# Performance work log

Hardware: AMD Instinct MI355X
Metric: run time of the kernel (lower is better)

The kernel has to match this reference:

```python
import jax, jax.numpy as jnp
import numpy as np

N_NODES = 100_000
M_EDGES = 500_000
F = 128       # elem_fea_len
H = 3         # elem_heads
HD = 256      # hidden layer dim of gate/message nets
BN_EPS = 1e-5


def setup_inputs() -> dict:
    key = jax.random.key(0)
    ks = jax.random.split(key, 12)
    s = 0.05
    return {
        "elem_weights": jax.random.uniform(ks[0], (N_NODES, 1), jnp.float32, 0.05, 1.0),
        "elem_in_fea": jax.random.normal(ks[1], (N_NODES, F), jnp.float32),
        "gate_W1": jax.random.normal(ks[2], (H, 2 * F, HD), jnp.float32) * s,
        "gate_b1": jnp.zeros((H, HD), jnp.float32),
        "gate_g": jnp.ones((H, HD), jnp.float32),
        "gate_beta": jnp.zeros((H, HD), jnp.float32),
        "gate_Wo": jax.random.normal(ks[3], (H, HD, 1), jnp.float32) * s,
        "gate_bo": jnp.zeros((H, 1), jnp.float32),
        "msg_W1": jax.random.normal(ks[4], (H, 2 * F, HD), jnp.float32) * s,
        "msg_b1": jnp.zeros((H, HD), jnp.float32),
        "msg_g": jnp.ones((H, HD), jnp.float32),
        "msg_beta": jnp.zeros((H, HD), jnp.float32),
        "msg_Wo": jax.random.normal(ks[5], (H, HD, F), jnp.float32) * s,
        "msg_bo": jnp.zeros((H, F), jnp.float32),
        "pow_p": jax.random.normal(ks[6], (H, 1), jnp.float32),
        "self_fea_idx": jax.random.randint(ks[7], (M_EDGES,), 0, N_NODES, jnp.int32),
        "nbr_fea_idx": jax.random.randint(ks[8], (M_EDGES,), 0, N_NODES, jnp.int32),
    }


def _simple_net(x, W1, b1, g, beta, Wo, bo):
    # Linear -> BatchNorm1d (training-mode batch stats) -> SiLU -> Linear
    h = x @ W1 + b1
    mu = jnp.mean(h, axis=0)
    var = jnp.mean(jnp.square(h - mu), axis=0)  # biased var, as torch BN
    h = (h - mu) * jax.lax.rsqrt(var + BN_EPS) * g + beta
    h = jax.nn.silu(h)
    return h @ Wo + bo


def reference(elem_weights, elem_in_fea, gate_W1, gate_b1, gate_g, gate_beta,
              gate_Wo, gate_bo, msg_W1, msg_b1, msg_g, msg_beta, msg_Wo,
              msg_bo, pow_p, self_fea_idx, nbr_fea_idx):
    n = elem_in_fea.shape[0]
    # gather edge endpoint features: (M, 2F)
    fea = jnp.concatenate([elem_in_fea[self_fea_idx], elem_in_fea[nbr_fea_idx]], axis=1)
    w = elem_weights[nbr_fea_idx]  # (M, 1)

    def head(gW1, gb1, gg, gbe, gWo, gbo, mW1, mb1, mg, mbe, mWo, mbo, p):
        gate = _simple_net(fea, gW1, gb1, gg, gbe, gWo, gbo)          # (M, 1)
        gmax = jax.ops.segment_max(gate, self_fea_idx, num_segments=n)
        gate = (w ** p) * jnp.exp(gate - gmax[self_fea_idx])
        den = jax.ops.segment_sum(gate, self_fea_idx, num_segments=n)
        gate = gate / (den[self_fea_idx] + 1e-10)
        msg = _simple_net(fea, mW1, mb1, mg, mbe, mWo, mbo)           # (M, F)
        return jax.ops.segment_sum(gate * msg, self_fea_idx, num_segments=n)

    head_out = jax.vmap(head)(gate_W1, gate_b1, gate_g, gate_beta, gate_Wo,
                              gate_bo, msg_W1, msg_b1, msg_g, msg_beta,
                              msg_Wo, msg_bo, pow_p)                  # (H, N, F)
    return jnp.mean(head_out, axis=0) + elem_in_fea
```

## Files before the change

### kernel.cpp

```cpp
#include <hip/hip_runtime.h>
#include <stdint.h>

#define NN 100000
#define MM 500000
#define FD 128
#define KK 256
#define NHEADS 3
#define NTILES 3907

typedef __attribute__((ext_vector_type(8))) __bf16 bf16x8;
typedef __attribute__((ext_vector_type(4))) float floatx4;

__device__ __forceinline__ float bf2f(unsigned short u) {
    union { uint32_t i; float f; } c; c.i = ((uint32_t)u) << 16; return c.f;
}
__device__ __forceinline__ unsigned short f2bf(float f) {
    union { float f; uint32_t i; } c; c.f = f;
    uint32_t i = c.i;
    return (unsigned short)((i + 0x7FFFu + ((i >> 16) & 1u)) >> 16);
}
__device__ __forceinline__ unsigned short f2bf_hw(float f) {
    __bf16 h = (__bf16)f;
    return __builtin_bit_cast(unsigned short, h);
}
__device__ __forceinline__ float silu(float a) { return a / (1.f + __expf(-a)); }
__device__ __forceinline__ float fin(float v) {
    return (v == v && fabsf(v) < 1e30f) ? v : 0.f;
}

__global__ void k_zero(float* __restrict__ p, int nwords) {
    int i = blockIdx.x * 256 + threadIdx.x;
    if (i < nwords) p[i] = 0.f;
}

__global__ void k_castx(const float* __restrict__ x, unsigned short* __restrict__ xb) {
    int i = blockIdx.x * 256 + threadIdx.x;
    if (i < NN * FD / 2) {
        float2 v = ((const float2*)x)[i];
        uint32_t p = (uint32_t)f2bf(v.x) | ((uint32_t)f2bf(v.y) << 16);
        ((uint32_t*)xb)[i] = p;
    }
}

__global__ void k_transpose_w1(const float* __restrict__ gw1,
                               const float* __restrict__ mw1,
                               unsigned short* __restrict__ W1t) {
    int idx = blockIdx.x * 256 + threadIdx.x;
    int j = idx >> 16;
    int rem = idx & 65535;
    int n = rem >> 8, k = rem & 255;
    const float* src = (j < 3) ? (gw1 + (size_t)j * 65536)
                               : (mw1 + (size_t)(j - 3) * 65536);
    W1t[(size_t)idx] = f2bf(src[k * 256 + n]);
}
__global__ void k_transpose_wo(const float* __restrict__ mwo,
                               unsigned short* __restrict__ Wot) {
    int idx = blockIdx.x * 256 + threadIdx.x;
    int h = idx / 32768;
    int rem = idx % 32768;
    int f = rem >> 8, k = rem & 255;
    Wot[idx] = f2bf(mwo[(size_t)h * 32768 + k * 128 + f]);
}

__global__ void k_hist(const int* __restrict__ idx, int* __restrict__ cnt) {
    int e = blockIdx.x * 256 + threadIdx.x;
    if (e < MM) atomicAdd(&cnt[idx[e]], 1);
}
__global__ void k_scan1(const int* __restrict__ cnt, int* __restrict__ pincl, int* __restrict__ bsum) {
    __shared__ int s[256];
    int t = threadIdx.x;
    int i = blockIdx.x * 256 + t;
    int v = (i < NN) ? cnt[i] : 0;
    s[t] = v; __syncthreads();
    for (int o = 1; o < 256; o <<= 1) {
        int add = (t >= o) ? s[t - o] : 0;
        __syncthreads();
        s[t] += add;
        __syncthreads();
    }
    if (i < NN) pincl[i] = s[t];
    if (t == 255) bsum[blockIdx.x] = s[255];
}
__global__ void k_scan2(const int* __restrict__ bsum, int* __restrict__ boff, int nb) {
    __shared__ int s[512];
    int t = threadIdx.x;
    int v = (t < nb) ? bsum[t] : 0;
    s[t] = v; __syncthreads();
    for (int o = 1; o < 512; o <<= 1) {
        int add = (t >= o) ? s[t - o] : 0;
        __syncthreads();
        s[t] += add;
        __syncthreads();
    }
    if (t < nb) boff[t] = s[t] - v;
}
__global__ void k_scan3(const int* __restrict__ pincl, const int* __restrict__ boff, int* __restrict__ rp) {
    int i = blockIdx.x * 256 + threadIdx.x;
    if (i < NN) rp[i + 1] = pincl[i] + boff[i >> 8];
    if (i == 0) rp[0] = 0;
}
__global__ void k_scatter(const int* __restrict__ self, const int* __restrict__ rp,
                          int* __restrict__ fill, int* __restrict__ elist) {
    int e = blockIdx.x * 256 + threadIdx.x;
    if (e < MM) {
        int n = self[e];
        int pos = atomicAdd(&fill[n], 1);
        elist[rp[n] + pos] = e;
    }
}
__global__ void k_perm(const int* __restrict__ elist, const int* __restrict__ self,
                       const int* __restrict__ nbr, int* __restrict__ selfp, int* __restrict__ nbrp) {
    int i = blockIdx.x * 256 + threadIdx.x;
    if (i < MM) {
        int e = elist[i];
        selfp[i] = self[e];
        nbrp[i] = nbr[e];
    }
}

__global__ void k_colsum(const float* __restrict__ x,
                         const int* __restrict__ cnt_self, const int* __restrict__ cnt_nbr,
                         float* __restrict__ colsum) {
    int t = threadIdx.x;
    int col = t & 127, part = t >> 7;
    const int* cp = part ? cnt_nbr : cnt_self;
    int n0 = blockIdx.x * 512;
    float a = 0.f;
    for (int i = 0; i < 512; i++) {
        int n = n0 + i;
        if (n < NN) {
            float c = (float)cp[n];
            a += c * x[(size_t)n * FD + col];
        }
    }
    atomicAdd(&colsum[part * 128 + col], a);
}

#define NCH 7813
#define CPB 62
__global__ __launch_bounds__(256, 2)
void k_S(const unsigned short* __restrict__ xb,
         const int* __restrict__ self_idx, const int* __restrict__ nbr_idx,
         float* __restrict__ S) {
    __shared__ unsigned short LT[256][72];
    const int tid = threadIdx.x;
    const int e_l = tid & 63;
    const int half = tid >> 6;
    const int ti = blockIdx.y >> 1, tj = blockIdx.y & 1;
    const int lane = tid & 63, w = tid >> 6;
    const int lr = lane & 15, q = lane >> 4;

    int cbeg = blockIdx.x * CPB;
    int cend = cbeg + CPB; if (cend > NCH) cend = NCH;

    floatx4 acc[2][8];
#pragma unroll
    for (int a = 0; a < 2; a++)
#pragma unroll
        for (int b = 0; b < 8; b++)
#pragma unroll
            for (int r = 0; r < 4; r++) acc[a][b][r] = 0.f;

    for (int ch = cbeg; ch < cend; ch++) {
        int e = ch * 64 + e_l;
        union { uint4 v[8]; unsigned short us[64]; } buf;
        if (e < MM) {
            int node = (half < 2) ? self_idx[e] : nbr_idx[e];
            const unsigned short* src = xb + (size_t)node * FD + (half & 1) * 64;
#pragma unroll
            for (int u2 = 0; u2 < 8; u2++) buf.v[u2] = *(const uint4*)(src + u2 * 8);
        } else {
#pragma unroll
            for (int u2 = 0; u2 < 8; u2++) { buf.v[u2].x = 0u; buf.v[u2].y = 0u; buf.v[u2].z = 0u; buf.v[u2].w = 0u; }
        }
        __syncthreads();
#pragma unroll
        for (int j2 = 0; j2 < 64; j2++)
            LT[half * 64 + j2][e_l] = buf.us[j2];
        __syncthreads();
#pragma unroll
        for (int ks = 0; ks < 64; ks += 32) {
            bf16x8 aF[2], bF[8];
#pragma unroll
            for (int mi = 0; mi < 2; mi++)
                aF[mi] = *(const bf16x8*)&LT[ti * 128 + w * 32 + mi * 16 + lr][ks + q * 8];
#pragma unroll
            for (int nj = 0; nj < 8; nj++)
                bF[nj] = *(const bf16x8*)&LT[tj * 128 + nj * 16 + lr][ks + q * 8];
#pragma unroll
            for (int mi = 0; mi < 2; mi++)
#pragma unroll
                for (int nj = 0; nj < 8; nj++)
                    acc[mi][nj] = __builtin_amdgcn_mfma_f32_16x16x32_bf16(aF[mi], bF[nj], acc[mi][nj], 0, 0, 0);
        }
    }
#pragma unroll
    for (int mi = 0; mi < 2; mi++)
#pragma unroll
        for (int nj = 0; nj < 8; nj++)
#pragma unroll
            for (int r = 0; r < 4; r++) {
                int row = ti * 128 + w * 32 + mi * 16 + q * 4 + r;
                int col = tj * 128 + nj * 16 + lr;
                atomicAdd(&S[row * 256 + col], acc[mi][nj][r]);
            }
}

__global__ void k_stats(const float* __restrict__ S, const float* __restrict__ colsum,
                        const unsigned short* __restrict__ W1t,
                        const float* __restrict__ gg, const float* __restrict__ gbe,
                        const float* __restrict__ mg, const float* __restrict__ mbe,
                        float* __restrict__ scaleA, float* __restrict__ shiftA) {
    __shared__ float ws[16][257];
    __shared__ float qq[16], uu[16];
    int t = threadIdx.x;
    int j = blockIdx.y;
    int c0 = blockIdx.x * 16;
    const unsigned short* Wn = W1t + (size_t)j * 65536;
    const float* g    = (j < 3) ? gg + j * 256 : mg + (j - 3) * 256;
    const float* beta = (j < 3) ? gbe + j * 256 : mbe + (j - 3) * 256;
#pragma unroll
    for (int i = 0; i < 16; i++) ws[i][t] = bf2f(Wn[(size_t)(c0 + i) * 256 + t]);
    if (t < 16) { qq[t] = 0.f; uu[t] = 0.f; }
    __syncthreads();
    float vpart[16];
#pragma unroll
    for (int i = 0; i < 16; i++) vpart[i] = 0.f;
    for (int k = 0; k < 256; k++) {
        float s = S[k * 256 + t];
#pragma unroll
        for (int i = 0; i < 16; i++) vpart[i] += s * ws[i][k];
    }
    float cs = colsum[t];
    int lane = t & 63;
#pragma unroll
    for (int i = 0; i < 16; i++) {
        float q1 = ws[i][t] * vpart[i];
        float u1 = cs * ws[i][t];
#pragma unroll
        for (int m = 1; m <= 32; m <<= 1) { q1 += __shfl_xor(q1, m); u1 += __shfl_xor(u1, m); }
        if (lane == 0) { atomicAdd(&qq[i], q1); atomicAdd(&uu[i], u1); }
    }
    __syncthreads();
    if (t < 16) {
        int c = c0 + t;
        float mu = fin(uu[t] / (float)MM);
        float var = fmaxf(fin(qq[t] / (float)MM - mu * mu), 0.f);
        float sc = fin(g[c] * rsqrtf(var + 1e-5f));
        scaleA[j * 256 + c] = sc;
        shiftA[j * 256 + c] = fin(beta[c] - mu * sc);
    }
}

__global__ __launch_bounds__(256, 2)
void k_gate(const unsigned short* __restrict__ x,
            const int* __restrict__ selfp, const int* __restrict__ nbrp,
            const unsigned short* __restrict__ W1t,
            const float* __restrict__ scale, const float* __restrict__ shift,
            const float* __restrict__ wo, const float* __restrict__ bo,
            float* __restrict__ glog) {
    __shared__ unsigned short As[128][72];
    __shared__ unsigned short Bs[128][72];
    __shared__ float sc[3][256], sh[3][256], wv[3][256];

    const int tid = threadIdx.x;
    const int m0 = blockIdx.x * 128;
#pragma unroll
    for (int h = 0; h < 3; h++) {
        sc[h][tid] = scale[h * 256 + tid];
        sh[h][tid] = shift[h * 256 + tid];
        wv[h][tid] = wo[h * 256 + tid];
    }
    __syncthreads();

    const int lane = tid & 63, w = tid >> 6;
    const int lr = lane & 15, q = lane >> 4;
    const int r0 = tid >> 1, hf = tid & 1;

    const int e0 = m0 + r0;
    const bool ein = e0 < MM;
    const int nodeS = ein ? selfp[e0] : 0;
    const int nodeN = ein ? nbrp[e0] : 0;
    const unsigned short* srcS = x + (size_t)nodeS * FD;
    const unsigned short* srcN = x + (size_t)nodeN * FD;

    for (int h = 0; h < 3; h++) {
        const unsigned short* W1h = W1t + (size_t)h * 65536;
        float dotp[2][4];
#pragma unroll
        for (int mi = 0; mi < 2; mi++)
#pragma unroll
            for (int r = 0; r < 4; r++) dotp[mi][r] = 0.f;

        for (int nh = 0; nh < 2; nh++) {
            floatx4 acc[2][8];
#pragma unroll
            for (int a = 0; a < 2; a++)
#pragma unroll
                for (int b = 0; b < 8; b++)
#pragma unroll
                    for (int r = 0; r < 4; r++) acc[a][b][r] = 0.f;

            for (int kc = 0; kc < 4; kc++) {
                {
                    const unsigned short* src = ((kc < 2) ? srcS : srcN) + (kc & 1) * 64 + hf * 32;
#pragma unroll
                    for (int u = 0; u < 4; u++)
                        *(uint4*)&As[r0][hf * 32 + u * 8] = *(const uint4*)(src + u * 8);
                }
                {
                    const unsigned short* src = W1h + (size_t)(nh * 128 + r0) * KK + kc * 64 + hf * 32;
#pragma unroll
                    for (int u = 0; u < 4; u++)
                        *(uint4*)&Bs[r0][hf * 32 + u * 8] = *(const uint4*)(src + u * 8);
                }
                __syncthreads();
#pragma unroll
                for (int ks = 0; ks < 64; ks += 32) {
                    bf16x8 aF[2], bF[8];
#pragma unroll
                    for (int mi = 0; mi < 2; mi++)
                        aF[mi] = *(const bf16x8*)&As[w * 32 + mi * 16 + lr][ks + q * 8];
#pragma unroll
                    for (int nj = 0; nj < 8; nj++)
                        bF[nj] = *(const bf16x8*)&Bs[nj * 16 + lr][ks + q * 8];
#pragma unroll
                    for (int mi = 0; mi < 2; mi++)
#pragma unroll
                        for (int nj = 0; nj < 8; nj++)
                            acc[mi][nj] = __builtin_amdgcn_mfma_f32_16x16x32_bf16(aF[mi], bF[nj], acc[mi][nj], 0, 0, 0);
                }
                __syncthreads();
            }
#pragma unroll
            for (int mi = 0; mi < 2; mi++)
#pragma unroll
                for (int r = 0; r < 4; r++) {
                    float d = 0.f;
#pragma unroll
                    for (int nj = 0; nj < 8; nj++) {
                        int cg = nh * 128 + nj * 16 + lr;
                        float v = acc[mi][nj][r] * sc[h][cg] + sh[h][cg];
                        d += silu(v) * wv[h][cg];
                    }
                    dotp[mi][r] += d;
                }
        }
        float b0 = bo[h];
#pragma unroll
        for (int mi = 0; mi < 2; mi++)
#pragma unroll
            for (int r = 0; r < 4; r++) {
                float v = dotp[mi][r];
                v += __shfl_xor(v, 1); v += __shfl_xor(v, 2);
                v += __shfl_xor(v, 4); v += __shfl_xor(v, 8);
                if (lr == 0) {
                    int row = w * 32 + mi * 16 + q * 4 + r;
                    int e = m0 + row;
                    if (e < MM) glog[(size_t)h * MM + e] = fin(v + b0);
                }
            }
    }
}

__global__ void k_coef(const int* __restrict__ rp, const float* __restrict__ glog,
                       float* __restrict__ coef, const float* __restrict__ ew,
                       const int* __restrict__ nbrp, const float* __restrict__ powp) {
    int n = blockIdx.x * 256 + threadIdx.x;
    if (n >= NN) return;
    int b = rp[n], e = rp[n + 1];
    if (e <= b) return;
    for (int h = 0; h < NHEADS; h++) {
        const float* gl = glog + (size_t)h * MM;
        float* cf = coef + (size_t)h * MM;
        float p = powp[h];
        float gmax = -3.4e38f;
        for (int i = b; i < e; i++) gmax = fmaxf(gmax, gl[i]);
        float den = 0.f;
        for (int i = b; i < e; i++) {
            float wv = ew[nbrp[i]];
            float u = fin(powf(wv, p) * __expf(gl[i] - gmax));
            cf[i] = u; den += u;
        }
        float inv = fin(1.f / (den + 1e-10f));
        for (int i = b; i < e; i++) cf[i] = fin(cf[i] * inv);
    }
}

__global__ __launch_bounds__(256, 2)
void k_msg(const unsigned short* __restrict__ x,
           const int* __restrict__ selfp, const int* __restrict__ nbrp,
           const unsigned short* __restrict__ W1t,
           const float* __restrict__ scale, const float* __restrict__ shift,
           const unsigned short* __restrict__ Wo2t,
           const float* __restrict__ bo2,
           const float* __restrict__ coef,
           float* __restrict__ out_acc) {
    __shared__ unsigned short As[128][72];
    __shared__ unsigned short Bs[128][72];
    __shared__ unsigned short ActC[128][72];
    __shared__ float sc[3][256], sh[3][256];
    __shared__ float bvec[3][128], cfs[3][128];
    __shared__ int nid[128];

    const int tid = threadIdx.x;
    const int m0 = blockIdx.x * 128;
#pragma unroll
    for (int h = 0; h < 3; h++) {
        sc[h][tid] = scale[h * 256 + tid];
        sh[h][tid] = shift[h * 256 + tid];
    }
    if (tid < 128) {
        int e = m0 + tid;
        nid[tid] = (e < MM) ? selfp[e] : -1;
#pragma unroll
        for (int h = 0; h < 3; h++) {
            bvec[h][tid] = bo2[h * 128 + tid];
            cfs[h][tid] = (e < MM) ? coef[(size_t)h * MM + e] : 0.f;
        }
    }
    __syncthreads();

    const int lane = tid & 63, w = tid >> 6;
    const int lr = lane & 15, q = lane >> 4;
    const int r0 = tid >> 1, hf = tid & 1;

    const int e0 = m0 + r0;
    const bool ein = e0 < MM;
    const int nodeS = ein ? selfp[e0] : 0;
    const int nodeN = ein ? nbrp[e0] : 0;
    const unsigned short* srcS = x + (size_t)nodeS * FD;
    const unsigned short* srcN = x + (size_t)nodeN * FD;

    floatx4 acc2[2][8];
#pragma unroll
    for (int a = 0; a < 2; a++)
#pragma unroll
        for (int b = 0; b < 8; b++)
#pragma unroll
            for (int r = 0; r < 4; r++) acc2[a][b][r] = 0.f;

    for (int h = 0; h < 3; h++) {
        const unsigned short* W1h = W1t + (size_t)h * 65536;
        const unsigned short* Wo2h = Wo2t + (size_t)h * 32768;
        float cfr[2][4];
#pragma unroll
        for (int mi = 0; mi < 2; mi++)
#pragma unroll
            for (int r = 0; r < 4; r++) cfr[mi][r] = cfs[h][w * 32 + mi * 16 + q * 4 + r];

        for (int nh = 0; nh < 2; nh++) {
            floatx4 acc[2][8];
#pragma unroll
            for (int a = 0; a < 2; a++)
#pragma unroll
                for (int b = 0; b < 8; b++)
#pragma unroll
                    for (int r = 0; r < 4; r++) acc[a][b][r] = 0.f;

            for (int kc = 0; kc < 4; kc++) {
                {
                    const unsigned short* src = ((kc < 2) ? srcS : srcN) + (kc & 1) * 64 + hf * 32;
#pragma unroll
                    for (int u = 0; u < 4; u++)
                        *(uint4*)&As[r0][hf * 32 + u * 8] = *(const uint4*)(src + u * 8);
                }
                {
                    const unsigned short* src = W1h + (size_t)(nh * 128 + r0) * KK + kc * 64 + hf * 32;
#pragma unroll
                    for (int u = 0; u < 4; u++)
                        *(uint4*)&Bs[r0][hf * 32 + u * 8] = *(const uint4*)(src + u * 8);
                }
                __syncthreads();
#pragma unroll
                for (int ks = 0; ks < 64; ks += 32) {
                    bf16x8 aF[2], bF[8];
#pragma unroll
                    for (int mi = 0; mi < 2; mi++)
                        aF[mi] = *(const bf16x8*)&As[w * 32 + mi * 16 + lr][ks + q * 8];
#pragma unroll
                    for (int nj = 0; nj < 8; nj++)
                        bF[nj] = *(const bf16x8*)&Bs[nj * 16 + lr][ks + q * 8];
#pragma unroll
                    for (int mi = 0; mi < 2; mi++)
#pragma unroll
                        for (int nj = 0; nj < 8; nj++)
                            acc[mi][nj] = __builtin_amdgcn_mfma_f32_16x16x32_bf16(aF[mi], bF[nj], acc[mi][nj], 0, 0, 0);
                }
                __syncthreads();
            }
            for (int kc2 = 0; kc2 < 2; kc2++) {
#pragma unroll
                for (int mi = 0; mi < 2; mi++)
#pragma unroll
                    for (int njl = 0; njl < 4; njl++)
#pragma unroll
                        for (int r = 0; r < 4; r++) {
                            int nj = kc2 * 4 + njl;
                            int row = w * 32 + mi * 16 + q * 4 + r;
                            int cg = nh * 128 + nj * 16 + lr;
                            float v = acc[mi][nj][r] * sc[h][cg] + sh[h][cg];
                            ActC[row][njl * 16 + lr] = f2bf_hw(silu(v) * cfr[mi][r]);
                        }
                {
                    const unsigned short* src = Wo2h + (size_t)r0 * KK + nh * 128 + kc2 * 64 + hf * 32;
#pragma unroll
                    for (int u = 0; u < 4; u++)
                        *(uint4*)&Bs[r0][hf * 32 + u * 8] = *(const uint4*)(src + u * 8);
                }
                __syncthreads();
#pragma unroll
                for (int ks = 0; ks < 64; ks += 32) {
                    bf16x8 aF[2], bF[8];
#pragma unroll
                    for (int mi = 0; mi < 2; mi++)
                        aF[mi] = *(const bf16x8*)&ActC[w * 32 + mi * 16 + lr][ks + q * 8];
#pragma unroll
                    for (int nj = 0; nj < 8; nj++)
                        bF[nj] = *(const bf16x8*)&Bs[nj * 16 + lr][ks + q * 8];
#pragma unroll
                    for (int mi = 0; mi < 2; mi++)
#pragma unroll
                        for (int nj = 0; nj < 8; nj++)
                            acc2[mi][nj] = __builtin_amdgcn_mfma_f32_16x16x32_bf16(aF[mi], bF[nj], acc2[mi][nj], 0, 0, 0);
                }
                __syncthreads();
            }
        }
    }
#pragma unroll
    for (int mi = 0; mi < 2; mi++) {
        int rbase = w * 32 + mi * 16 + q * 4;
        int n0 = nid[rbase], n3 = nid[rbase + 3];
        float c0[3], c1[3], c2[3], c3[3];
#pragma unroll
        for (int h = 0; h < 3; h++) {
            c0[h] = cfs[h][rbase];     c1[h] = cfs[h][rbase + 1];
            c2[h] = cfs[h][rbase + 2]; c3[h] = cfs[h][rbase + 3];
        }
#pragma unroll
        for (int nj = 0; nj < 8; nj++) {
            int col = nj * 16 + lr;
            float b0h = bvec[0][col], b1h = bvec[1][col], b2h = bvec[2][col];
            float v0 = acc2[mi][nj][0] + c0[0] * b0h + c0[1] * b1h + c0[2] * b2h;
            float v1 = acc2[mi][nj][1] + c1[0] * b0h + c1[1] * b1h + c1[2] * b2h;
            float v2 = acc2[mi][nj][2] + c2[0] * b0h + c2[1] * b1h + c2[2] * b2h;
            float v3 = acc2[mi][nj][3] + c3[0] * b0h + c3[1] * b1h + c3[2] * b2h;
            if (n0 == n3) {
                if (n0 >= 0) atomicAdd(&out_acc[(size_t)n0 * FD + col], v0 + v1 + v2 + v3);
            } else {
                int n1 = nid[rbase + 1], n2 = nid[rbase + 2];
                if (n0 >= 0) atomicAdd(&out_acc[(size_t)n0 * FD + col], v0);
                if (n1 >= 0) atomicAdd(&out_acc[(size_t)n1 * FD + col], v1);
                if (n2 >= 0) atomicAdd(&out_acc[(size_t)n2 * FD + col], v2);
                if (n3 >= 0) atomicAdd(&out_acc[(size_t)n3 * FD + col], v3);
            }
        }
    }
}

__global__ void k_finalout(float* __restrict__ out, const float* __restrict__ x) {
    int i = blockIdx.x * 256 + threadIdx.x;
    if (i < NN * FD) out[i] = fin(out[i]) * (1.f / 3.f) + x[i];
}

extern "C" void kernel_launch(void* const* d_in, const int* in_sizes, int n_in,
                              void* d_out, int out_size, void* d_ws, size_t ws_size,
                              hipStream_t stream) {
    const float* ew   = (const float*)d_in[0];
    const float* x    = (const float*)d_in[1];
    const float* gW1  = (const float*)d_in[2];
    const float* gg   = (const float*)d_in[4];
    const float* gbe  = (const float*)d_in[5];
    const float* gWo  = (const float*)d_in[6];
    const float* gbo  = (const float*)d_in[7];
    const float* mW1  = (const float*)d_in[8];
    const float* mg   = (const float*)d_in[10];
    const float* mbe  = (const float*)d_in[11];
    const float* mWo  = (const float*)d_in[12];
    const float* mbo  = (const float*)d_in[13];
    const float* powp = (const float*)d_in[14];
    const int* self_idx = (const int*)d_in[15];
    const int* nbr_idx  = (const int*)d_in[16];
    float* out = (float*)d_out;

    char* ws = (char*)d_ws;
    size_t off = 0;
    auto alloc = [&](size_t bytes) -> void* {
        size_t o = off;
        off += (bytes + 255) & ~(size_t)255;
        return (void*)(ws + o);
    };

    float* S       = (float*)alloc(256 * 256 * 4);
    float* colsum  = (float*)alloc(512 * 4);
    int*   cnt     = (int*)alloc((size_t)NN * 4);
    int*   cntn    = (int*)alloc((size_t)NN * 4);
    int*   fill    = (int*)alloc((size_t)NN * 4);
    size_t zero_end = off;
    unsigned short* xb   = (unsigned short*)alloc((size_t)NN * FD * 2);
    unsigned short* W1t  = (unsigned short*)alloc(6ull * 65536 * 2);
    unsigned short* Wo2t = (unsigned short*)alloc(3ull * 32768 * 2);
    float* scaleA = (float*)alloc(6ull * 256 * 4);
    float* shiftA = (float*)alloc(6ull * 256 * 4);
    int*   rp     = (int*)alloc((size_t)(NN + 1) * 4);
    int*   pincl  = (int*)alloc((size_t)NN * 4);
    int*   bsum   = (int*)alloc(512 * 4);
    int*   boff   = (int*)alloc(512 * 4);
    int*   elist  = (int*)alloc((size_t)MM * 4);
    int*   selfp  = (int*)alloc((size_t)MM * 4);
    int*   nbrp   = (int*)alloc((size_t)MM * 4);
    float* glog   = (float*)alloc(3ull * MM * 4);
    float* coef   = (float*)alloc(3ull * MM * 4);
    if (off > ws_size) return;

    int zwords = (int)(zero_end / 4);
    k_zero<<<(zwords + 255) / 256, 256, 0, stream>>>(S, zwords);
    k_zero<<<(NN * FD + 255) / 256, 256, 0, stream>>>(out, NN * FD);

    k_castx<<<(NN * FD / 2 + 255) / 256, 256, 0, stream>>>(x, xb);
    k_transpose_w1<<<1536, 256, 0, stream>>>(gW1, mW1, W1t);
    k_transpose_wo<<<384, 256, 0, stream>>>(mWo, Wo2t);

    k_hist<<<1954, 256, 0, stream>>>(self_idx, cnt);
    k_hist<<<1954, 256, 0, stream>>>(nbr_idx, cntn);
    int nb1 = (NN + 255) / 256;
    k_scan1<<<nb1, 256, 0, stream>>>(cnt, pincl, bsum);
    k_scan2<<<1, 512, 0, stream>>>(bsum, boff, nb1);
    k_scan3<<<nb1, 256, 0, stream>>>(pincl, boff, rp);
    k_scatter<<<1954, 256, 0, stream>>>(self_idx, rp, fill, elist);
    k_perm<<<1954, 256, 0, stream>>>(elist, self_idx, nbr_idx, selfp, nbrp);

    k_colsum<<<(NN + 511) / 512, 256, 0, stream>>>(x, cnt, cntn, colsum);
    k_S<<<dim3(128, 4), 256, 0, stream>>>(xb, self_idx, nbr_idx, S);
    k_stats<<<dim3(16, 6), 256, 0, stream>>>(S, colsum, W1t, gg, gbe, mg, mbe, scaleA, shiftA);

    k_gate<<<NTILES, 256, 0, stream>>>(xb, selfp, nbrp, W1t,
                                       scaleA, shiftA, gWo, gbo, glog);
    k_coef<<<nb1, 256, 0, stream>>>(rp, glog, coef, ew, nbrp, powp);
    k_msg<<<NTILES, 256, 0, stream>>>(xb, selfp, nbrp, W1t + 3ull * 65536,
                                      scaleA + 3 * 256, shiftA + 3 * 256,
                                      Wo2t, mbo, coef, out);
    k_finalout<<<(NN * FD + 255) / 256, 256, 0, stream>>>(out, x);
}
```

Before: 1.771 ms.

## Double-buffer weight tiles via direct global-to-LDS loads and keep gathered A in registers

```diff
diff --git a/kernel.cpp b/kernel.cpp
--- a/kernel.cpp
+++ b/kernel.cpp
@@ -26,6 +26,14 @@
 __device__ __forceinline__ float silu(float a) { return a / (1.f + __expf(-a)); }
 __device__ __forceinline__ float fin(float v) {
     return (v == v && fabsf(v) < 1e30f) ? v : 0.f;
+}
+__device__ __forceinline__ void gl_lds16(const void* g, void* l) {
+    __builtin_amdgcn_global_load_lds(
+        (const __attribute__((address_space(1))) unsigned int*)g,
+        (__attribute__((address_space(3))) unsigned int*)l, 16, 0, 0);
+}
+__device__ __forceinline__ void vm_drain() {
+    asm volatile("s_waitcnt vmcnt(0)" ::: "memory");
 }
 
 __global__ void k_zero(float* __restrict__ p, int nwords) {
@@ -259,9 +267,9 @@
             const float* __restrict__ scale, const float* __restrict__ shift,
             const float* __restrict__ wo, const float* __restrict__ bo,
             float* __restrict__ glog) {
-    __shared__ unsigned short As[128][72];
-    __shared__ unsigned short Bs[128][72];
+    __shared__ unsigned char Bs[2][16384];
     __shared__ float sc[3][256], sh[3][256], wv[3][256];
+    __shared__ int nid[128], nidN[128];
 
     const int tid = threadIdx.x;
     const int m0 = blockIdx.x * 128;
@@ -271,21 +279,53 @@
         sh[h][tid] = shift[h * 256 + tid];
         wv[h][tid] = wo[h * 256 + tid];
     }
+    if (tid < 128) {
+        int e = m0 + tid;
+        nid[tid]  = (e < MM) ? selfp[e] : 0;
+        nidN[tid] = (e < MM) ? nbrp[e] : 0;
+    }
     __syncthreads();
 
     const int lane = tid & 63, w = tid >> 6;
     const int lr = lane & 15, q = lane >> 4;
-    const int r0 = tid >> 1, hf = tid & 1;
-
-    const int e0 = m0 + r0;
-    const bool ein = e0 < MM;
-    const int nodeS = ein ? selfp[e0] : 0;
-    const int nodeN = ein ? nbrp[e0] : 0;
-    const unsigned short* srcS = x + (size_t)nodeS * FD;
-    const unsigned short* srcN = x + (size_t)nodeN * FD;
-
+    const int swz = (lr & 7) << 4;
+
+    bf16x8 aReg[2][8];
+    {
+        const unsigned short* bS0 = x + (size_t)nid[w * 32 + lr] * FD;
+        const unsigned short* bS1 = x + (size_t)nid[w * 32 + 16 + lr] * FD;
+        const unsigned short* bN0 = x + (size_t)nidN[w * 32 + lr] * FD;
+        const unsigned short* bN1 = x + (size_t)nidN[w * 32 + 16 + lr] * FD;
+#pragma unroll
+        for (int s = 0; s < 8; s++) {
+            int koff = (s & 3) * 32 + q * 8;
+            aReg[0][s] = *(const bf16x8*)(((s < 4) ? bS0 : bN0) + koff);
+            aReg[1][s] = *(const bf16x8*)(((s < 4) ? bS1 : bN1) + koff);
+        }
+    }
+
+    uint32_t pre[4];
+#pragma unroll
+    for (int c = 0; c < 4; c++) {
+        int o = (w * 4 + c) * 1024 + lane * 16;
+        int r = o >> 7, lc = o & 127;
+        pre[c] = (uint32_t)(r * 512 + (lc ^ ((r & 7) << 4)));
+    }
+
+    auto STAGE = [&](int t, int b) {
+        int hh = t >> 3, rr = t & 7, nh2 = rr >> 2, kc = rr & 3;
+        const char* gb = (const char*)(W1t + (size_t)hh * 65536 + (size_t)nh2 * 32768 + kc * 64);
+#pragma unroll
+        for (int c = 0; c < 4; c++)
+            gl_lds16(gb + pre[c], &Bs[b][(w * 4 + c) * 1024]);
+    };
+
+    STAGE(0, 0);
+    vm_drain();
+    __syncthreads();
+
+    int buf = 0, tcur = 0;
     for (int h = 0; h < 3; h++) {
-        const unsigned short* W1h = W1t + (size_t)h * 65536;
         float dotp[2][4];
 #pragma unroll
         for (int mi = 0; mi < 2; mi++)
@@ -301,36 +341,26 @@
 #pragma unroll
                     for (int r = 0; r < 4; r++) acc[a][b][r] = 0.f;
 
+#pragma unroll
             for (int kc = 0; kc < 4; kc++) {
-                {
-                    const unsigned short* src = ((kc < 2) ? srcS : srcN) + (kc & 1) * 64 + hf * 32;
-#pragma unroll
-                    for (int u = 0; u < 4; u++)
-                        *(uint4*)&As[r0][hf * 32 + u * 8] = *(const uint4*)(src + u * 8);
+                if (tcur + 1 < 24) STAGE(tcur + 1, buf ^ 1);
+#pragma unroll
+                for (int ks = 0; ks < 2; ks++) {
+                    bf16x8 bF[8];
+#pragma unroll
+                    for (int nj = 0; nj < 8; nj++)
+                        bF[nj] = *(const bf16x8*)&Bs[buf][(nj * 16 + lr) * 128 + ((ks * 64 + q * 16) ^ swz)];
+                    __builtin_amdgcn_s_setprio(1);
+#pragma unroll
+                    for (int mi = 0; mi < 2; mi++)
+#pragma unroll
+                        for (int nj = 0; nj < 8; nj++)
+                            acc[mi][nj] = __builtin_amdgcn_mfma_f32_16x16x32_bf16(aReg[mi][kc * 2 + ks], bF[nj], acc[mi][nj], 0, 0, 0);
+                    __builtin_amdgcn_s_setprio(0);
                 }
-                {
-                    const unsigned short* src = W1h + (size_t)(nh * 128 + r0) * KK + kc * 64 + hf * 32;
-#pragma unroll
-                    for (int u = 0; u < 4; u++)
-                        *(uint4*)&Bs[r0][hf * 32 + u * 8] = *(const uint4*)(src + u * 8);
-                }
+                vm_drain();
                 __syncthreads();
-#pragma unroll
-                for (int ks = 0; ks < 64; ks += 32) {
-                    bf16x8 aF[2], bF[8];
-#pragma unroll
-                    for (int mi = 0; mi < 2; mi++)
-                        aF[mi] = *(const bf16x8*)&As[w * 32 + mi * 16 + lr][ks + q * 8];
-#pragma unroll
-                    for (int nj = 0; nj < 8; nj++)
-                        bF[nj] = *(const bf16x8*)&Bs[nj * 16 + lr][ks + q * 8];
-#pragma unroll
-                    for (int mi = 0; mi < 2; mi++)
-#pragma unroll
-                        for (int nj = 0; nj < 8; nj++)
-                            acc[mi][nj] = __builtin_amdgcn_mfma_f32_16x16x32_bf16(aF[mi], bF[nj], acc[mi][nj], 0, 0, 0);
-                }
-                __syncthreads();
+                buf ^= 1; tcur++;
             }
 #pragma unroll
             for (int mi = 0; mi < 2; mi++)
@@ -396,12 +426,11 @@
            const float* __restrict__ bo2,
            const float* __restrict__ coef,
            float* __restrict__ out_acc) {
-    __shared__ unsigned short As[128][72];
-    __shared__ unsigned short Bs[128][72];
+    __shared__ unsigned char Bs[2][16384];
     __shared__ unsigned short ActC[128][72];
     __shared__ float sc[3][256], sh[3][256];
     __shared__ float bvec[3][128], cfs[3][128];
-    __shared__ int nid[128];
+    __shared__ int nid[128], nidN[128];
 
     const int tid = threadIdx.x;
     const int m0 = blockIdx.x * 128;
@@ -412,7 +441,8 @@
     }
     if (tid < 128) {
         int e = m0 + tid;
-        nid[tid] = (e < MM) ? selfp[e] : -1;
+        nid[tid]  = (e < MM) ? selfp[e] : -1;
+        nidN[tid] = (e < MM) ? nbrp[e] : 0;
 #pragma unroll
         for (int h = 0; h < 3; h++) {
             bvec[h][tid] = bo2[h * 128 + tid];
@@ -423,14 +453,46 @@
 
     const int lane = tid & 63, w = tid >> 6;
     const int lr = lane & 15, q = lane >> 4;
-    const int r0 = tid >> 1, hf = tid & 1;
-
-    const int e0 = m0 + r0;
-    const bool ein = e0 < MM;
-    const int nodeS = ein ? selfp[e0] : 0;
-    const int nodeN = ein ? nbrp[e0] : 0;
-    const unsigned short* srcS = x + (size_t)nodeS * FD;
-    const unsigned short* srcN = x + (size_t)nodeN * FD;
+    const int swz = (lr & 7) << 4;
+
+    bf16x8 aReg[2][8];
+    {
+        int nS0 = nid[w * 32 + lr];      if (nS0 < 0) nS0 = 0;
+        int nS1 = nid[w * 32 + 16 + lr]; if (nS1 < 0) nS1 = 0;
+        const unsigned short* bS0 = x + (size_t)nS0 * FD;
+        const unsigned short* bS1 = x + (size_t)nS1 * FD;
+        const unsigned short* bN0 = x + (size_t)nidN[w * 32 + lr] * FD;
+        const unsigned short* bN1 = x + (size_t)nidN[w * 32 + 16 + lr] * FD;
+#pragma unroll
+        for (int s = 0; s < 8; s++) {
+            int koff = (s & 3) * 32 + q * 8;
+            aReg[0][s] = *(const bf16x8*)(((s < 4) ? bS0 : bN0) + koff);
+            aReg[1][s] = *(const bf16x8*)(((s < 4) ? bS1 : bN1) + koff);
+        }
+    }
+
+    uint32_t pre[4];
+#pragma unroll
+    for (int c = 0; c < 4; c++) {
+        int o = (w * 4 + c) * 1024 + lane * 16;
+        int r = o >> 7, lc = o & 127;
+        pre[c] = (uint32_t)(r * 512 + (lc ^ ((r & 7) << 4)));
+    }
+
+    auto STAGE = [&](int t, int b) {
+        int hh = t / 12, rr = t % 12, nh2 = rr / 6, s6 = rr % 6;
+        const unsigned short* base = (s6 < 4)
+            ? (W1t + (size_t)hh * 65536 + (size_t)nh2 * 32768 + s6 * 64)
+            : (Wo2t + (size_t)hh * 32768 + nh2 * 128 + (s6 - 4) * 64);
+        const char* gb = (const char*)base;
+#pragma unroll
+        for (int c = 0; c < 4; c++)
+            gl_lds16(gb + pre[c], &Bs[b][(w * 4 + c) * 1024]);
+    };
+
+    STAGE(0, 0);
+    vm_drain();
+    __syncthreads();
 
     floatx4 acc2[2][8];
 #pragma unroll
@@ -440,9 +502,8 @@
 #pragma unroll
             for (int r = 0; r < 4; r++) acc2[a][b][r] = 0.f;
 
+    int buf = 0, tcur = 0;
     for (int h = 0; h < 3; h++) {
-        const unsigned short* W1h = W1t + (size_t)h * 65536;
-        const unsigned short* Wo2h = Wo2t + (size_t)h * 32768;
         float cfr[2][4];
 #pragma unroll
         for (int mi = 0; mi < 2; mi++)
@@ -458,38 +519,30 @@
 #pragma unroll
                     for (int r = 0; r < 4; r++) acc[a][b][r] = 0.f;
 
+#pragma unroll
             for (int kc = 0; kc < 4; kc++) {
-                {
-                    const unsigned short* src = ((kc < 2) ? srcS : srcN) + (kc & 1) * 64 + hf * 32;
-#pragma unroll
-                    for (int u = 0; u < 4; u++)
-                        *(uint4*)&As[r0][hf * 32 + u * 8] = *(const uint4*)(src + u * 8);
+                if (tcur + 1 < 36) STAGE(tcur + 1, buf ^ 1);
+#pragma unroll
+                for (int ks = 0; ks < 2; ks++) {
+                    bf16x8 bF[8];
+#pragma unroll
+                    for (int nj = 0; nj < 8; nj++)
+                        bF[nj] = *(const bf16x8*)&Bs[buf][(nj * 16 + lr) * 128 + ((ks * 64 + q * 16) ^ swz)];
+                    __builtin_amdgcn_s_setprio(1);
+#pragma unroll
+                    for (int mi = 0; mi < 2; mi++)
+#pragma unroll
+                        for (int nj = 0; nj < 8; nj++)
+                            acc[mi][nj] = __builtin_amdgcn_mfma_f32_16x16x32_bf16(aReg[mi][kc * 2 + ks], bF[nj], acc[mi][nj], 0, 0, 0);
+                    __builtin_amdgcn_s_setprio(0);
                 }
-                {
-                    const unsigned short* src = W1h + (size_t)(nh * 128 + r0) * KK + kc * 64 + hf * 32;
-#pragma unroll
-                    for (int u = 0; u < 4; u++)
-                        *(uint4*)&Bs[r0][hf * 32 + u * 8] = *(const uint4*)(src + u * 8);
-                }
+                vm_drain();
                 __syncthreads();
-#pragma unroll
-                for (int ks = 0; ks < 64; ks += 32) {
-                    bf16x8 aF[2], bF[8];
-#pragma unroll
-                    for (int mi = 0; mi < 2; mi++)
-                        aF[mi] = *(const bf16x8*)&As[w * 32 + mi * 16 + lr][ks + q * 8];
-#pragma unroll
-                    for (int nj = 0; nj < 8; nj++)
-                        bF[nj] = *(const bf16x8*)&Bs[nj * 16 + lr][ks + q * 8];
-#pragma unroll
-                    for (int mi = 0; mi < 2; mi++)
-#pragma unroll
-                        for (int nj = 0; nj < 8; nj++)
-                            acc[mi][nj] = __builtin_amdgcn_mfma_f32_16x16x32_bf16(aF[mi], bF[nj], acc[mi][nj], 0, 0, 0);
-                }
-                __syncthreads();
+                buf ^= 1; tcur++;
             }
+#pragma unroll
             for (int kc2 = 0; kc2 < 2; kc2++) {
+                if (tcur + 1 < 36) STAGE(tcur + 1, buf ^ 1);
 #pragma unroll
                 for (int mi = 0; mi < 2; mi++)
 #pragma unroll
@@ -502,29 +555,26 @@
                             float v = acc[mi][nj][r] * sc[h][cg] + sh[h][cg];
                             ActC[row][njl * 16 + lr] = f2bf_hw(silu(v) * cfr[mi][r]);
                         }
-                {
-                    const unsigned short* src = Wo2h + (size_t)r0 * KK + nh * 128 + kc2 * 64 + hf * 32;
-#pragma unroll
-                    for (int u = 0; u < 4; u++)
-                        *(uint4*)&Bs[r0][hf * 32 + u * 8] = *(const uint4*)(src + u * 8);
-                }
-                __syncthreads();
-#pragma unroll
-                for (int ks = 0; ks < 64; ks += 32) {
+#pragma unroll
+                for (int ks = 0; ks < 2; ks++) {
                     bf16x8 aF[2], bF[8];
 #pragma unroll
                     for (int mi = 0; mi < 2; mi++)
-                        aF[mi] = *(const bf16x8*)&ActC[w * 32 + mi * 16 + lr][ks + q * 8];
+                        aF[mi] = *(const bf16x8*)&ActC[w * 32 + mi * 16 + lr][ks * 32 + q * 8];
 #pragma unroll
                     for (int nj = 0; nj < 8; nj++)
-                        bF[nj] = *(const bf16x8*)&Bs[nj * 16 + lr][ks + q * 8];
+                        bF[nj] = *(const bf16x8*)&Bs[buf][(nj * 16 + lr) * 128 + ((ks * 64 + q * 16) ^ swz)];
+                    __builtin_amdgcn_s_setprio(1);
 #pragma unroll
                     for (int mi = 0; mi < 2; mi++)
 #pragma unroll
                         for (int nj = 0; nj < 8; nj++)
                             acc2[mi][nj] = __builtin_amdgcn_mfma_f32_16x16x32_bf16(aF[mi], bF[nj], acc2[mi][nj], 0, 0, 0);
+                    __builtin_amdgcn_s_setprio(0);
                 }
+                vm_drain();
                 __syncthreads();
+                buf ^= 1; tcur++;
             }
         }
     }
```

Result: faster. 1.616 ms (-8.7%).
